# Kernel tuning notes

Hardware: AMD Instinct MI355X
Metric: run time of the kernel (lower is better)

## Reference

```python
import jax, jax.numpy as jnp
import numpy as np

B, TE, TD, H = 8, 512, 256, 256  # batch, enc len, dec len, hidden (He==Hd)

def setup_inputs() -> dict:
    key = jax.random.key(0)
    k1, k2, k3, k4, k5 = jax.random.split(key, 5)
    # Keras 'uniform' initializer: U(-0.05, 0.05)
    u = lambda k, s: jax.random.uniform(k, s, jnp.float32, -0.05, 0.05)
    return {
        "encoder_out_seq": jax.random.normal(k1, (B, TE, H), jnp.float32),
        "decoder_out_seq": jax.random.normal(k2, (B, TD, H), jnp.float32),
        "W_a": u(k3, (H, H)),
        "U_a": u(k4, (H, H)),
        "V_a": u(k5, (H, 1)),
    }

def reference(encoder_out_seq, decoder_out_seq, W_a, U_a, V_a):
    # Bahdanau additive attention, fully batched (same math as the per-step K.rnn loop)
    We = jnp.einsum('bih,hk->bik', encoder_out_seq, W_a)   # [B,Te,H]
    Uh = jnp.einsum('bjh,hk->bjk', decoder_out_seq, U_a)   # [B,Td,H]
    # energies: V_a^T tanh(We_i + Uh_j)  -> [B,Td,Te]
    t = jnp.tanh(We[:, None, :, :] + Uh[:, :, None, :])    # [B,Td,Te,H]
    e = jnp.einsum('bjih,h->bji', t, V_a[:, 0])             # [B,Td,Te]
    e = jax.nn.softmax(e, axis=-1)                          # softmax over encoder positions
    c = jnp.einsum('bji,bih->bjh', e, encoder_out_seq)      # [B,Td,H]
    return (c, e)
```

## Files before the change

kernel.cpp:

```cpp
#include <hip/hip_runtime.h>


#define BB 8
#define TE 512
#define TD 256
#define HH 256

#define EXP2F(x) __builtin_amdgcn_exp2f(x)
#define RCPF(x)  __builtin_amdgcn_rcpf(x)
#define KSCALE   2.8853900817779268f
#define NSC      (-2.8853900817779268f)

__global__ __launch_bounds__(256) void k_pre(
    const float* __restrict__ enc, const float* __restrict__ dec,
    const float* __restrict__ Wa,  const float* __restrict__ Ua,
    float* __restrict__ W4, float* __restrict__ Uhe)
{
    const int tid = threadIdx.x;
    const bool is_enc = blockIdx.x < 256;
    const int bi = is_enc ? blockIdx.x : (blockIdx.x - 256);
    const int m0 = (bi >> 2) * 64;
    const int n0 = (bi & 3) * 64;
    const float* X = is_enc ? enc : dec;
    const float* W = is_enc ? Wa : Ua;

    __shared__ float Xs[32][68];
    __shared__ float Ws[32][68];

    const int kq = tid & 7,  xr = tid >> 3;
    const int wk = tid >> 3, wn = (tid & 7) * 8;
    const int tx = tid & 15, ty = tid >> 4;

    float acc[4][4];
    #pragma unroll
    for (int r = 0; r < 4; r++)
        #pragma unroll
        for (int c = 0; c < 4; c++) acc[r][c] = 0.f;

    for (int kc = 0; kc < HH; kc += 32) {
        float4 xa = *(const float4*)(X + (size_t)(m0 + xr) * HH + kc + kq * 4);
        float4 xb = *(const float4*)(X + (size_t)(m0 + xr + 32) * HH + kc + kq * 4);
        float4 wa = *(const float4*)(W + (size_t)(kc + wk) * HH + n0 + wn);
        float4 wb = *(const float4*)(W + (size_t)(kc + wk) * HH + n0 + wn + 4);
        __syncthreads();
        Xs[kq * 4 + 0][xr] = xa.x; Xs[kq * 4 + 1][xr] = xa.y;
        Xs[kq * 4 + 2][xr] = xa.z; Xs[kq * 4 + 3][xr] = xa.w;
        Xs[kq * 4 + 0][xr + 32] = xb.x; Xs[kq * 4 + 1][xr + 32] = xb.y;
        Xs[kq * 4 + 2][xr + 32] = xb.z; Xs[kq * 4 + 3][xr + 32] = xb.w;
        *(float4*)&Ws[wk][wn]     = wa;
        *(float4*)&Ws[wk][wn + 4] = wb;
        __syncthreads();
        #pragma unroll
        for (int k = 0; k < 32; k++) {
            float4 a = *(const float4*)&Xs[k][ty * 4];
            float4 b = *(const float4*)&Ws[k][tx * 4];
            acc[0][0] = fmaf(a.x, b.x, acc[0][0]); acc[0][1] = fmaf(a.x, b.y, acc[0][1]);
            acc[0][2] = fmaf(a.x, b.z, acc[0][2]); acc[0][3] = fmaf(a.x, b.w, acc[0][3]);
            acc[1][0] = fmaf(a.y, b.x, acc[1][0]); acc[1][1] = fmaf(a.y, b.y, acc[1][1]);
            acc[1][2] = fmaf(a.y, b.z, acc[1][2]); acc[1][3] = fmaf(a.y, b.w, acc[1][3]);
            acc[2][0] = fmaf(a.z, b.x, acc[2][0]); acc[2][1] = fmaf(a.z, b.y, acc[2][1]);
            acc[2][2] = fmaf(a.z, b.z, acc[2][2]); acc[2][3] = fmaf(a.z, b.w, acc[2][3]);
            acc[3][0] = fmaf(a.w, b.x, acc[3][0]); acc[3][1] = fmaf(a.w, b.y, acc[3][1]);
            acc[3][2] = fmaf(a.w, b.z, acc[3][2]); acc[3][3] = fmaf(a.w, b.w, acc[3][3]);
        }
    }

    if (is_enc) {
        const int b  = m0 >> 9;
        const int ib = (m0 & 511) + ty * 4;
        const int hq = (n0 >> 2) + tx;
        float* dst = W4 + (((size_t)b * 64 + hq) * TE + ib) * 4;
        #pragma unroll
        for (int r = 0; r < 4; r++) {
            float4 v;
            v.x = EXP2F(acc[r][0] * KSCALE); v.y = EXP2F(acc[r][1] * KSCALE);
            v.z = EXP2F(acc[r][2] * KSCALE); v.w = EXP2F(acc[r][3] * KSCALE);
            *(float4*)(dst + (size_t)r * 4) = v;
        }
    } else {
        #pragma unroll
        for (int r = 0; r < 4; r++) {
            float4 v;
            v.x = EXP2F(acc[r][0] * KSCALE); v.y = EXP2F(acc[r][1] * KSCALE);
            v.z = EXP2F(acc[r][2] * KSCALE); v.w = EXP2F(acc[r][3] * KSCALE);
            *(float4*)(Uhe + (size_t)(m0 + ty * 4 + r) * HH + n0 + tx * 4) = v;
        }
    }
}

__global__ __launch_bounds__(512) void k_attn(
    const float* __restrict__ enc, const float* __restrict__ W4,
    const float* __restrict__ Uhe, const float* __restrict__ Va,
    float* __restrict__ out_c, float* __restrict__ out_e)
{
    const int wv = threadIdx.x >> 6, lane = threadIdx.x & 63;
    const int b   = blockIdx.x & 7;
    const int j0  = (blockIdx.x >> 3) * 4;
    const int jj0 = b * TD + j0;

    __shared__ float sP[4][TE];
    __shared__ float sR[8][4][HH];

    const int i = (wv << 6) + lane;
    const float* wp = W4 + ((size_t)b * 64 * TE + i) * 4;
    const float* ua = Uhe + (size_t)jj0 * HH;
    const float* va = Va;

    float a0 = 0.f, a1 = 0.f, a2 = 0.f, a3 = 0.f;

#define QSTEP(ACC, U)                                                     \
    {                                                                     \
        float A_ = fmaf(w4.x, (U).x, 1.f);                                \
        float B_ = fmaf(w4.y, (U).y, 1.f);                                \
        float C_ = fmaf(w4.z, (U).z, 1.f);                                \
        float D_ = fmaf(w4.w, (U).w, 1.f);                                \
        float dAB = A_ * B_, dCD = C_ * D_;                               \
        float nAB = fmaf(v4.x, B_, v4.y * A_);                            \
        float nCD = fmaf(v4.z, D_, v4.w * C_);                            \
        float num = fmaf(nAB, dCD, nCD * dAB);                            \
        ACC = fmaf(num, RCPF(dAB * dCD), ACC);                            \
    }

    #pragma unroll 2
    for (int q = 0; q < 64; q++) {
        float4 w4 = *(const float4*)(wp + (size_t)q * TE * 4);
        float4 v4 = *(const float4*)(va + 4 * q);
        float4 u0 = *(const float4*)(ua + 4 * q);
        float4 u1 = *(const float4*)(ua + HH + 4 * q);
        float4 u2 = *(const float4*)(ua + 2 * HH + 4 * q);
        float4 u3 = *(const float4*)(ua + 3 * HH + 4 * q);
        QSTEP(a0, u0)
        QSTEP(a1, u1)
        QSTEP(a2, u2)
        QSTEP(a3, u3)
    }
#undef QSTEP

    sP[0][i] = NSC * a0;
    sP[1][i] = NSC * a1;
    sP[2][i] = NSC * a2;
    sP[3][i] = NSC * a3;
    __syncthreads();

    if (wv < 4) {
        float ev[8];
        float m = -3.0e38f;
        #pragma unroll
        for (int k = 0; k < 8; k++) {
            ev[k] = sP[wv][lane + 64 * k];
            m = fmaxf(m, ev[k]);
        }
        #pragma unroll
        for (int off = 32; off; off >>= 1) m = fmaxf(m, __shfl_xor(m, off, 64));
        float s = 0.f;
        #pragma unroll
        for (int k = 0; k < 8; k++) { ev[k] = EXP2F(ev[k] - m); s += ev[k]; }
        #pragma unroll
        for (int off = 32; off; off >>= 1) s += __shfl_xor(s, off, 64);
        float rs = RCPF(s);
        float* oe = out_e + (size_t)(jj0 + wv) * TE;
        #pragma unroll
        for (int k = 0; k < 8; k++) {
            float p = ev[k] * rs;
            sP[wv][lane + 64 * k] = p;
            oe[lane + 64 * k] = p;
        }
    }
    __syncthreads();

    const int ib = wv << 6;
    const float* eb = enc + ((size_t)b * TE + ib) * HH + 4 * lane;
    float4 c0 = {0,0,0,0}, c1 = {0,0,0,0}, c2 = {0,0,0,0}, c3 = {0,0,0,0};
    #pragma unroll 2
    for (int k = 0; k < 64; k++) {
        float p0 = sP[0][ib + k];
        float p1 = sP[1][ib + k];
        float p2 = sP[2][ib + k];
        float p3 = sP[3][ib + k];
        float4 q = *(const float4*)(eb + (size_t)k * HH);
        c0.x = fmaf(p0, q.x, c0.x); c0.y = fmaf(p0, q.y, c0.y);
        c0.z = fmaf(p0, q.z, c0.z); c0.w = fmaf(p0, q.w, c0.w);
        c1.x = fmaf(p1, q.x, c1.x); c1.y = fmaf(p1, q.y, c1.y);
        c1.z = fmaf(p1, q.z, c1.z); c1.w = fmaf(p1, q.w, c1.w);
        c2.x = fmaf(p2, q.x, c2.x); c2.y = fmaf(p2, q.y, c2.y);
        c2.z = fmaf(p2, q.z, c2.z); c2.w = fmaf(p2, q.w, c2.w);
        c3.x = fmaf(p3, q.x, c3.x); c3.y = fmaf(p3, q.y, c3.y);
        c3.z = fmaf(p3, q.z, c3.z); c3.w = fmaf(p3, q.w, c3.w);
    }
    *(float4*)&sR[wv][0][4 * lane] = c0;
    *(float4*)&sR[wv][1][4 * lane] = c1;
    *(float4*)&sR[wv][2][4 * lane] = c2;
    *(float4*)&sR[wv][3][4 * lane] = c3;
    __syncthreads();

    {
        const int jr = wv & 3;
        const int h2 = (wv >> 2) * 128 + 2 * lane;
        float sx = 0.f, sy = 0.f;
        #pragma unroll
        for (int ww = 0; ww < 8; ww++) {
            float2 t = *(const float2*)&sR[ww][jr][h2];
            sx += t.x; sy += t.y;
        }
        float2 o; o.x = sx; o.y = sy;
        *(float2*)(out_c + (size_t)(jj0 + jr) * HH + h2) = o;
    }
}

extern "C" void kernel_launch(void* const* d_in, const int* in_sizes, int n_in,
                              void* d_out, int out_size, void* d_ws, size_t ws_size,
                              hipStream_t stream) {
    const float* enc = (const float*)d_in[0];
    const float* dec = (const float*)d_in[1];
    const float* Wa  = (const float*)d_in[2];
    const float* Ua  = (const float*)d_in[3];
    const float* Va  = (const float*)d_in[4];

    float* W4  = (float*)d_ws;
    float* Uhe = W4 + (size_t)BB * HH * TE;

    float* out_c = (float*)d_out;
    float* out_e = out_c + (size_t)BB * TD * HH;

    k_pre<<<384, 256, 0, stream>>>(enc, dec, Wa, Ua, W4, Uhe);
    k_attn<<<BB * TD / 4, 512, 0, stream>>>(enc, W4, Uhe, Va, out_c, out_e);
}
```

Before: 113.8 us.

## Use split-bf16 MFMA for projection GEMMs with pre-transposed weight kernel

Replaces the FP32 FMA tiled GEMM in k_pre with bf16 MFMA 16x16x32 instructions, using a hi/lo split (three MFMAs) to keep near-FP32 accuracy. A new k_tw kernel transposes W_a/U_a and splits them into bf16 hi/lo halves in workspace. Activations are split on the fly and register-prefetched one K-chunk ahead. This adds an extra kernel launch and some precision loss from the three-term split, while the dominant attention kernel is unchanged.

```diff
diff --git a/kernel.cpp b/kernel.cpp
--- a/kernel.cpp
+++ b/kernel.cpp
@@ -11,79 +11,161 @@
 #define KSCALE   2.8853900817779268f
 #define NSC      (-2.8853900817779268f)
 
+typedef __attribute__((ext_vector_type(8))) short short8_t;
+typedef __attribute__((ext_vector_type(4))) float f32x4;
+
+__device__ __forceinline__ unsigned short f2bf(float x) {
+    unsigned int u = __float_as_uint(x);
+    return (unsigned short)((u + 0x7FFFu + ((u >> 16) & 1u)) >> 16);
+}
+__device__ __forceinline__ float bf2f(unsigned short h) {
+    return __uint_as_float(((unsigned int)h) << 16);
+}
+
+__global__ __launch_bounds__(256) void k_tw(
+    const float* __restrict__ Wa, const float* __restrict__ Ua,
+    unsigned short* __restrict__ Wth, unsigned short* __restrict__ Wtl)
+{
+    const int t    = threadIdx.x;
+    const int s    = blockIdx.x >> 4;
+    const int tile = blockIdx.x & 15;
+    const int tk   = (tile >> 2) * 64;
+    const int th   = (tile & 3) * 64;
+    const float* W = s ? Ua : Wa;
+
+    __shared__ float Ls[64][65];
+    const int kr = t >> 4;
+    const int hc = (t & 15) * 4;
+    #pragma unroll
+    for (int r = 0; r < 4; r++) {
+        float4 v = *(const float4*)(W + (size_t)(tk + kr + 16 * r) * HH + th + hc);
+        Ls[kr + 16 * r][hc + 0] = v.x; Ls[kr + 16 * r][hc + 1] = v.y;
+        Ls[kr + 16 * r][hc + 2] = v.z; Ls[kr + 16 * r][hc + 3] = v.w;
+    }
+    __syncthreads();
+    const int hr  = t >> 4;
+    const int kc4 = (t & 15) * 4;
+    #pragma unroll
+    for (int r = 0; r < 4; r++) {
+        const int hl = hr + 16 * r;
+        float f0 = Ls[kc4 + 0][hl], f1 = Ls[kc4 + 1][hl];
+        float f2 = Ls[kc4 + 2][hl], f3 = Ls[kc4 + 3][hl];
+        ushort4 hi, lo;
+        hi.x = f2bf(f0); lo.x = f2bf(f0 - bf2f(hi.x));
+        hi.y = f2bf(f1); lo.y = f2bf(f1 - bf2f(hi.y));
+        hi.z = f2bf(f2); lo.z = f2bf(f2 - bf2f(hi.z));
+        hi.w = f2bf(f3); lo.w = f2bf(f3 - bf2f(hi.w));
+        const size_t o = ((size_t)(s * 256 + th + hl)) * 256 + tk + kc4;
+        *(ushort4*)(Wth + o) = hi;
+        *(ushort4*)(Wtl + o) = lo;
+    }
+}
+
 __global__ __launch_bounds__(256) void k_pre(
     const float* __restrict__ enc, const float* __restrict__ dec,
-    const float* __restrict__ Wa,  const float* __restrict__ Ua,
+    const unsigned short* __restrict__ Wth, const unsigned short* __restrict__ Wtl,
     float* __restrict__ W4, float* __restrict__ Uhe)
 {
-    const int tid = threadIdx.x;
-    const bool is_enc = blockIdx.x < 256;
-    const int bi = is_enc ? blockIdx.x : (blockIdx.x - 256);
-    const int m0 = (bi >> 2) * 64;
-    const int n0 = (bi & 3) * 64;
-    const float* X = is_enc ? enc : dec;
-    const float* W = is_enc ? Wa : Ua;
-
-    __shared__ float Xs[32][68];
-    __shared__ float Ws[32][68];
-
-    const int kq = tid & 7,  xr = tid >> 3;
-    const int wk = tid >> 3, wn = (tid & 7) * 8;
-    const int tx = tid & 15, ty = tid >> 4;
-
-    float acc[4][4];
-    #pragma unroll
-    for (int r = 0; r < 4; r++)
-        #pragma unroll
-        for (int c = 0; c < 4; c++) acc[r][c] = 0.f;
-
-    for (int kc = 0; kc < HH; kc += 32) {
-        float4 xa = *(const float4*)(X + (size_t)(m0 + xr) * HH + kc + kq * 4);
-        float4 xb = *(const float4*)(X + (size_t)(m0 + xr + 32) * HH + kc + kq * 4);
-        float4 wa = *(const float4*)(W + (size_t)(kc + wk) * HH + n0 + wn);
-        float4 wb = *(const float4*)(W + (size_t)(kc + wk) * HH + n0 + wn + 4);
+    const int t  = threadIdx.x;
+    const int it = blockIdx.x >> 2;
+    const int ht = blockIdx.x & 3;
+    const int i0 = it * 64;
+    const int h0 = ht * 64;
+    const bool is_enc = (i0 < BB * TE);
+    const float* X = is_enc ? (enc + (size_t)i0 * HH)
+                            : (dec + (size_t)(i0 - BB * TE) * HH);
+    const int s = is_enc ? 0 : 1;
+    const unsigned short* Ah = Wth + ((size_t)(s * 256 + h0)) * 256;
+    const unsigned short* Al = Wtl + ((size_t)(s * 256 + h0)) * 256;
+
+    __shared__ unsigned short At_h[64][40], At_l[64][40];
+    __shared__ unsigned short Xs_h[64][40], Xs_l[64][40];
+
+    const int sr = t >> 2;
+    const int sq = (t & 3) * 8;
+
+    const int wv = t >> 6, l = t & 63;
+    const int wh = (wv & 1) * 32;
+    const int wi = (wv >> 1) * 32;
+    const int fr = l & 15;
+    const int fk = (l >> 4) * 8;
+    const int rq = l >> 4;
+
+    f32x4 acc[2][2];
+    #pragma unroll
+    for (int a0 = 0; a0 < 2; a0++)
+        #pragma unroll
+        for (int a1 = 0; a1 < 2; a1++)
+            acc[a0][a1] = (f32x4){0.f, 0.f, 0.f, 0.f};
+
+    short8_t aH = *(const short8_t*)(Ah + (size_t)sr * 256 + sq);
+    short8_t aL = *(const short8_t*)(Al + (size_t)sr * 256 + sq);
+    float4   x0 = *(const float4*)(X + (size_t)sr * HH + sq);
+    float4   x1 = *(const float4*)(X + (size_t)sr * HH + sq + 4);
+
+    #pragma unroll
+    for (int c = 0; c < 8; c++) {
+        short8_t xh, xl;
+        {
+            unsigned short h;
+            h = f2bf(x0.x); xh[0] = (short)h; xl[0] = (short)f2bf(x0.x - bf2f(h));
+            h = f2bf(x0.y); xh[1] = (short)h; xl[1] = (short)f2bf(x0.y - bf2f(h));
+            h = f2bf(x0.z); xh[2] = (short)h; xl[2] = (short)f2bf(x0.z - bf2f(h));
+            h = f2bf(x0.w); xh[3] = (short)h; xl[3] = (short)f2bf(x0.w - bf2f(h));
+            h = f2bf(x1.x); xh[4] = (short)h; xl[4] = (short)f2bf(x1.x - bf2f(h));
+            h = f2bf(x1.y); xh[5] = (short)h; xl[5] = (short)f2bf(x1.y - bf2f(h));
+            h = f2bf(x1.z); xh[6] = (short)h; xl[6] = (short)f2bf(x1.z - bf2f(h));
+            h = f2bf(x1.w); xh[7] = (short)h; xl[7] = (short)f2bf(x1.w - bf2f(h));
+        }
         __syncthreads();
-        Xs[kq * 4 + 0][xr] = xa.x; Xs[kq * 4 + 1][xr] = xa.y;
-        Xs[kq * 4 + 2][xr] = xa.z; Xs[kq * 4 + 3][xr] = xa.w;
-        Xs[kq * 4 + 0][xr + 32] = xb.x; Xs[kq * 4 + 1][xr + 32] = xb.y;
-        Xs[kq * 4 + 2][xr + 32] = xb.z; Xs[kq * 4 + 3][xr + 32] = xb.w;
-        *(float4*)&Ws[wk][wn]     = wa;
-        *(float4*)&Ws[wk][wn + 4] = wb;
+        *(short8_t*)&At_h[sr][sq] = aH;
+        *(short8_t*)&At_l[sr][sq] = aL;
+        *(short8_t*)&Xs_h[sr][sq] = xh;
+        *(short8_t*)&Xs_l[sr][sq] = xl;
+        if (c < 7) {
+            const int kc = (c + 1) * 32;
+            aH = *(const short8_t*)(Ah + (size_t)sr * 256 + kc + sq);
+            aL = *(const short8_t*)(Al + (size_t)sr * 256 + kc + sq);
+            x0 = *(const float4*)(X + (size_t)sr * HH + kc + sq);
+            x1 = *(const float4*)(X + (size_t)sr * HH + kc + sq + 4);
+        }
         __syncthreads();
         #pragma unroll
-        for (int k = 0; k < 32; k++) {
-            float4 a = *(const float4*)&Xs[k][ty * 4];
-            float4 b = *(const float4*)&Ws[k][tx * 4];
-            acc[0][0] = fmaf(a.x, b.x, acc[0][0]); acc[0][1] = fmaf(a.x, b.y, acc[0][1]);
-            acc[0][2] = fmaf(a.x, b.z, acc[0][2]); acc[0][3] = fmaf(a.x, b.w, acc[0][3]);
-            acc[1][0] = fmaf(a.y, b.x, acc[1][0]); acc[1][1] = fmaf(a.y, b.y, acc[1][1]);
-            acc[1][2] = fmaf(a.y, b.z, acc[1][2]); acc[1][3] = fmaf(a.y, b.w, acc[1][3]);
-            acc[2][0] = fmaf(a.z, b.x, acc[2][0]); acc[2][1] = fmaf(a.z, b.y, acc[2][1]);
-            acc[2][2] = fmaf(a.z, b.z, acc[2][2]); acc[2][3] = fmaf(a.z, b.w, acc[2][3]);
-            acc[3][0] = fmaf(a.w, b.x, acc[3][0]); acc[3][1] = fmaf(a.w, b.y, acc[3][1]);
-            acc[3][2] = fmaf(a.w, b.z, acc[3][2]); acc[3][3] = fmaf(a.w, b.w, acc[3][3]);
-        }
-    }
-
-    if (is_enc) {
-        const int b  = m0 >> 9;
-        const int ib = (m0 & 511) + ty * 4;
-        const int hq = (n0 >> 2) + tx;
-        float* dst = W4 + (((size_t)b * 64 + hq) * TE + ib) * 4;
-        #pragma unroll
-        for (int r = 0; r < 4; r++) {
-            float4 v;
-            v.x = EXP2F(acc[r][0] * KSCALE); v.y = EXP2F(acc[r][1] * KSCALE);
-            v.z = EXP2F(acc[r][2] * KSCALE); v.w = EXP2F(acc[r][3] * KSCALE);
-            *(float4*)(dst + (size_t)r * 4) = v;
-        }
-    } else {
-        #pragma unroll
-        for (int r = 0; r < 4; r++) {
-            float4 v;
-            v.x = EXP2F(acc[r][0] * KSCALE); v.y = EXP2F(acc[r][1] * KSCALE);
-            v.z = EXP2F(acc[r][2] * KSCALE); v.w = EXP2F(acc[r][3] * KSCALE);
-            *(float4*)(Uhe + (size_t)(m0 + ty * 4 + r) * HH + n0 + tx * 4) = v;
+        for (int fm = 0; fm < 2; fm++) {
+            short8_t a_h = *(const short8_t*)&At_h[wh + 16 * fm + fr][fk];
+            short8_t a_l = *(const short8_t*)&At_l[wh + 16 * fm + fr][fk];
+            #pragma unroll
+            for (int fn = 0; fn < 2; fn++) {
+                short8_t b_h = *(const short8_t*)&Xs_h[wi + 16 * fn + fr][fk];
+                short8_t b_l = *(const short8_t*)&Xs_l[wi + 16 * fn + fr][fk];
+                acc[fm][fn] = __builtin_amdgcn_mfma_f32_16x16x32_bf16(a_h, b_h, acc[fm][fn], 0, 0, 0);
+                acc[fm][fn] = __builtin_amdgcn_mfma_f32_16x16x32_bf16(a_h, b_l, acc[fm][fn], 0, 0, 0);
+                acc[fm][fn] = __builtin_amdgcn_mfma_f32_16x16x32_bf16(a_l, b_h, acc[fm][fn], 0, 0, 0);
+            }
+        }
+    }
+
+    #pragma unroll
+    for (int fm = 0; fm < 2; fm++) {
+        #pragma unroll
+        for (int fn = 0; fn < 2; fn++) {
+            f32x4 v = acc[fm][fn];
+            float4 o;
+            o.x = EXP2F(v[0] * KSCALE);
+            o.y = EXP2F(v[1] * KSCALE);
+            o.z = EXP2F(v[2] * KSCALE);
+            o.w = EXP2F(v[3] * KSCALE);
+            const int ig = i0 + wi + 16 * fn + fr;
+            const int hb = h0 + wh + 16 * fm + rq * 4;
+            if (is_enc) {
+                const int b  = ig >> 9;
+                const int ib = ig & 511;
+                const int hq = hb >> 2;
+                *(float4*)(W4 + (((size_t)b * 64 + hq) * TE + ib) * 4) = o;
+            } else {
+                const int j = ig - BB * TE;
+                *(float4*)(Uhe + (size_t)j * HH + hb) = o;
+            }
         }
     }
 }
@@ -218,10 +300,13 @@
 
     float* W4  = (float*)d_ws;
     float* Uhe = W4 + (size_t)BB * HH * TE;
+    unsigned short* Wth = (unsigned short*)(Uhe + (size_t)BB * TD * HH);
+    unsigned short* Wtl = Wth + 2 * 256 * 256;
 
     float* out_c = (float*)d_out;
     float* out_e = out_c + (size_t)BB * TD * HH;
 
-    k_pre<<<384, 256, 0, stream>>>(enc, dec, Wa, Ua, W4, Uhe);
+    k_tw<<<32, 256, 0, stream>>>(Wa, Ua, Wth, Wtl);
+    k_pre<<<384, 256, 0, stream>>>(enc, dec, Wth, Wtl, W4, Uhe);
     k_attn<<<BB * TD / 4, 512, 0, stream>>>(enc, W4, Uhe, Va, out_c, out_e);
 }
```

Result: faster. 107.9 us (-5.1%).
